# Kernel tuning notes

Measured on AMD Instinct MI355X. Metric: run time of the kernel, lower is better.

## Reference

```python
import jax, jax.numpy as jnp
import numpy as np

NUM_CLASSES = 4      # config.class_num (malaria stages)
N = 2048             # total nodes = source + target samples
S = 1024             # source_length
FEAT_IN = 25088      # VGG19 include_top=False -> 7*7*512 flattened
D_FC = 512           # Dense(512)
D_G1 = 512           # config.features_dim (GCNConv1 out)
D_G2 = 256           # config.GCN_hidderlayer_dim_num (GCNConv2 out)


def setup_inputs() -> dict:
    key = jax.random.key(0)
    ks = jax.random.split(key, 8)
    sc = lambda fan_in: np.float32(1.0 / np.sqrt(fan_in))
    return {
        "x": jax.random.normal(ks[0], (N, FEAT_IN), jnp.float32),
        "W_fc": jax.random.normal(ks[1], (FEAT_IN, D_FC), jnp.float32) * sc(FEAT_IN),
        "b_fc": jnp.zeros((D_FC,), jnp.float32),
        "W_g1": jax.random.normal(ks[2], (D_FC, D_G1), jnp.float32) * sc(D_FC),
        "b_g1": jnp.zeros((D_G1,), jnp.float32),
        "W_g2": jax.random.normal(ks[3], (D_G1, D_G2), jnp.float32) * sc(D_G1),
        "b_g2": jnp.zeros((D_G2,), jnp.float32),
        "source_labels": jax.random.randint(ks[4], (S,), 0, NUM_CLASSES),
        "source_length": S,
    }


def reference(x, W_fc, b_fc, W_g1, b_g1, W_g2, b_g2, source_labels, source_length):
    # fc after (omitted frozen) VGG19 backbone + flatten
    feats = x @ W_fc + b_fc                                   # [N, 512]

    # get_centers: per-class SUM of source features (no averaging, faithful)
    src = feats[:source_length]                               # [S, 512]
    centers = jax.ops.segment_sum(src, source_labels, num_segments=NUM_CLASSES)  # [C, 512]

    # per-target euclidean distance to each centroid + argmin
    # (argmin of squared distance == argmin of euclidean distance)
    tgt = feats[source_length:]                               # [T, 512]
    d2 = (jnp.sum(tgt * tgt, axis=1, keepdims=True)
          - 2.0 * (tgt @ centers.T)
          + jnp.sum(centers * centers, axis=1)[None, :])      # [T, C]
    target_labels = jnp.argmin(d2, axis=1)                    # [T] int

    # label-cluster graph: edge iff same label; source block forced to identity
    all_labels = jnp.concatenate([source_labels.astype(jnp.int32),
                                  target_labels.astype(jnp.int32)])
    adj = (all_labels[:, None] == all_labels[None, :]).astype(feats.dtype)  # [N, N]
    adj = adj.at[:source_length, :source_length].set(
        jnp.eye(source_length, dtype=feats.dtype))

    # add_self_loops(value=1) then symmetric gcn_filter D^-1/2 A D^-1/2
    A = adj + jnp.eye(N, dtype=feats.dtype)
    dinv = jax.lax.rsqrt(jnp.sum(A, axis=1))                  # [N]
    A_norm = dinv[:, None] * A * dinv[None, :]                # [N, N]

    # two GCN layers (spektral GCNConv: A_norm @ (X @ W) + b) with relu
    h = jax.nn.relu(A_norm @ (feats @ W_g1) + b_g1)           # [N, 512]
    h = jax.nn.relu(A_norm @ (h @ W_g2) + b_g2)               # [N, 256]
    return (h, A_norm, feats)
```

## Files before the change

kernel.cpp:

```cpp
#include <hip/hip_runtime.h>

#define NROWS 2048
#define SLEN  1024
#define FEAT  25088
#define DFC   512
#define DG1   512
#define DG2   256
#define CSPLIT 128

typedef __attribute__((ext_vector_type(8))) short short8;
typedef __attribute__((ext_vector_type(4))) float f32x4;

__device__ __forceinline__ unsigned short bfbits(float f) {
  unsigned int u = __float_as_uint(f);
  u += 0x7fffu + ((u >> 16) & 1u);
  return (unsigned short)(u >> 16);
}

__global__ void transpose_cvt_k(const float* __restrict__ src, unsigned short* __restrict__ dst,
                                int K, int Ncol) {
  __shared__ float tile[64][65];
  int kb = blockIdx.x * 64, nb = blockIdx.y * 64;
  int tx = threadIdx.x & 63, ty = threadIdx.x >> 6;
  #pragma unroll
  for (int i = ty; i < 64; i += 4)
    tile[i][tx] = src[(size_t)(kb + i) * Ncol + (nb + tx)];
  __syncthreads();
  #pragma unroll
  for (int i = ty; i < 64; i += 4)
    dst[(size_t)(nb + i) * K + (kb + tx)] = bfbits(tile[tx][i]);
}

template<bool AF32>
__global__ __launch_bounds__(256) void gemm_k(const void* __restrict__ Aptr,
    const unsigned short* __restrict__ BT, float* __restrict__ Cacc,
    int K, int Ncols, int tiles_n, int ksteps) {
  __shared__ unsigned short Al[128 * 40];
  __shared__ unsigned short Bl[128 * 40];
  int tid = threadIdx.x;
  int m0 = (blockIdx.x / tiles_n) * 128;
  int n0 = (blockIdx.x % tiles_n) * 128;
  int kbase = blockIdx.y * ksteps * 32;
  int wid = tid >> 6, lane = tid & 63;
  int wm = wid >> 1, wn = wid & 1;
  int lrow = lane & 15, lko = lane >> 4;

  f32x4 acc[4][4];
  #pragma unroll
  for (int i = 0; i < 4; i++)
    #pragma unroll
    for (int j = 0; j < 4; j++) acc[i][j] = (f32x4){0.f, 0.f, 0.f, 0.f};

  for (int t = 0; t < ksteps; ++t) {
    int k0 = kbase + t * 32;
    __syncthreads();
    if constexpr (AF32) {
      const float* A = (const float*)Aptr;
      #pragma unroll
      for (int i = 0; i < 4; i++) {
        int idx = tid + i * 256;
        int row = idx >> 3, kq = idx & 7;
        float4 v = *reinterpret_cast<const float4*>(A + (size_t)(m0 + row) * K + k0 + kq * 4);
        ushort4 u;
        u.x = bfbits(v.x); u.y = bfbits(v.y); u.z = bfbits(v.z); u.w = bfbits(v.w);
        *reinterpret_cast<ushort4*>(&Al[row * 40 + kq * 4]) = u;
      }
    } else {
      const unsigned short* A = (const unsigned short*)Aptr;
      #pragma unroll
      for (int i = 0; i < 2; i++) {
        int idx = tid + i * 256;
        int row = idx >> 2, kq = idx & 3;
        int4 v = *reinterpret_cast<const int4*>(A + (size_t)(m0 + row) * K + k0 + kq * 8);
        *reinterpret_cast<int4*>(&Al[row * 40 + kq * 8]) = v;
      }
    }
    #pragma unroll
    for (int i = 0; i < 2; i++) {
      int idx = tid + i * 256;
      int row = idx >> 2, kq = idx & 3;
      int4 v = *reinterpret_cast<const int4*>(BT + (size_t)(n0 + row) * K + k0 + kq * 8);
      *reinterpret_cast<int4*>(&Bl[row * 40 + kq * 8]) = v;
    }
    __syncthreads();
    short8 af[4], bfv[4];
    #pragma unroll
    for (int mi = 0; mi < 4; mi++)
      af[mi] = *reinterpret_cast<const short8*>(&Al[(wm * 64 + mi * 16 + lrow) * 40 + lko * 8]);
    #pragma unroll
    for (int ni = 0; ni < 4; ni++)
      bfv[ni] = *reinterpret_cast<const short8*>(&Bl[(wn * 64 + ni * 16 + lrow) * 40 + lko * 8]);
    #pragma unroll
    for (int mi = 0; mi < 4; mi++)
      #pragma unroll
      for (int ni = 0; ni < 4; ni++)
        acc[mi][ni] = __builtin_amdgcn_mfma_f32_16x16x32_bf16(af[mi], bfv[ni], acc[mi][ni], 0, 0, 0);
  }
  #pragma unroll
  for (int mi = 0; mi < 4; mi++)
    #pragma unroll
    for (int ni = 0; ni < 4; ni++)
      #pragma unroll
      for (int r = 0; r < 4; r++) {
        int row = m0 + wm * 64 + mi * 16 + lko * 4 + r;
        int col = n0 + wn * 64 + ni * 16 + lrow;
        atomicAdd(&Cacc[(size_t)row * Ncols + col], acc[mi][ni][r]);
      }
}

__global__ void feats_fin_k(const float* __restrict__ facc, const float* __restrict__ bfc,
                            float* __restrict__ outf, unsigned short* __restrict__ outbf) {
  int i = blockIdx.y;
  int n = blockIdx.x * 256 + threadIdx.x;
  float v = facc[(size_t)i * DFC + n] + bfc[n];
  outf[(size_t)i * DFC + n] = v;
  outbf[(size_t)i * DFC + n] = bfbits(v);
}

__global__ void seg_sum_part_k(const float* __restrict__ x, const int* __restrict__ slab,
                               float* __restrict__ sxp) {
  int k4 = blockIdx.x * 256 + threadIdx.x;
  if (k4 >= FEAT / 4) return;
  int k = k4 * 4;
  int i0 = blockIdx.y * 128, i1 = i0 + 128;
  float4 a0 = {0,0,0,0}, a1 = {0,0,0,0}, a2 = {0,0,0,0}, a3 = {0,0,0,0};
  #pragma unroll 4
  for (int i = i0; i < i1; i++) {
    float4 v = *reinterpret_cast<const float4*>(x + (size_t)i * FEAT + k);
    int c = slab[i];
    float m0 = (c == 0) ? 1.f : 0.f, m1 = (c == 1) ? 1.f : 0.f;
    float m2 = (c == 2) ? 1.f : 0.f, m3 = (c == 3) ? 1.f : 0.f;
    a0.x += m0 * v.x; a0.y += m0 * v.y; a0.z += m0 * v.z; a0.w += m0 * v.w;
    a1.x += m1 * v.x; a1.y += m1 * v.y; a1.z += m1 * v.z; a1.w += m1 * v.w;
    a2.x += m2 * v.x; a2.y += m2 * v.y; a2.z += m2 * v.z; a2.w += m2 * v.w;
    a3.x += m3 * v.x; a3.y += m3 * v.y; a3.z += m3 * v.z; a3.w += m3 * v.w;
  }
  size_t base = (size_t)blockIdx.y * 4 * FEAT;
  *reinterpret_cast<float4*>(sxp + base + 0 * FEAT + k) = a0;
  *reinterpret_cast<float4*>(sxp + base + 1 * FEAT + k) = a1;
  *reinterpret_cast<float4*>(sxp + base + 2 * FEAT + k) = a2;
  *reinterpret_cast<float4*>(sxp + base + 3 * FEAT + k) = a3;
}

__global__ void seg_sum_reduce_k(const float* __restrict__ sxp, float* __restrict__ sx) {
  int k4 = blockIdx.x * 256 + threadIdx.x;
  if (k4 >= FEAT / 4) return;
  int k = k4 * 4;
  int c = blockIdx.y;
  double s0 = 0, s1 = 0, s2 = 0, s3 = 0;
  #pragma unroll
  for (int p = 0; p < 8; p++) {
    float4 v = *reinterpret_cast<const float4*>(sxp + ((size_t)p * 4 + c) * FEAT + k);
    s0 += (double)v.x; s1 += (double)v.y; s2 += (double)v.z; s3 += (double)v.w;
  }
  float4 r; r.x = (float)s0; r.y = (float)s1; r.z = (float)s2; r.w = (float)s3;
  *reinterpret_cast<float4*>(sx + (size_t)c * FEAT + k) = r;
}

__global__ void count_src_k(const int* __restrict__ slab, int* __restrict__ cnt) {
  __shared__ int c[4];
  if (threadIdx.x < 4) c[threadIdx.x] = 0;
  __syncthreads();
  for (int i = threadIdx.x; i < SLEN; i += 256) atomicAdd(&c[slab[i]], 1);
  __syncthreads();
  if (threadIdx.x < 4) cnt[threadIdx.x] = c[threadIdx.x];
}

__global__ void centers_part_k(const float* __restrict__ sx, const float* __restrict__ W,
                               double* __restrict__ cpart) {
  int n = blockIdx.x * 64 + (threadIdx.x & 63);
  int cc = threadIdx.x >> 6;
  int kb = blockIdx.y * (FEAT / CSPLIT), ke = kb + FEAT / CSPLIT;
  const float* sr = sx + (size_t)cc * FEAT;
  double acc = 0.0;
  #pragma unroll 4
  for (int k = kb; k < ke; k++)
    acc += (double)sr[k] * (double)W[(size_t)k * DFC + n];
  cpart[((size_t)blockIdx.y * 4 + cc) * DFC + n] = acc;
}

__global__ void centers_reduce_k(const double* __restrict__ cpart, const float* __restrict__ bfc,
                                 const int* __restrict__ cntsrc, float* __restrict__ Cent) {
  int idx = blockIdx.x * 256 + threadIdx.x;
  int cc = idx >> 9, n = idx & 511;
  double s = 0.0;
  #pragma unroll 4
  for (int p = 0; p < CSPLIT; p++) s += cpart[((size_t)p * 4 + cc) * DFC + n];
  Cent[idx] = (float)(s + (double)cntsrc[cc] * (double)bfc[n]);
}

__global__ void wc_k(const float* __restrict__ W, const float* __restrict__ Cent,
                     float* __restrict__ wc) {
  __shared__ float cs[4 * DFC];
  for (int i = threadIdx.x; i < 4 * DFC; i += 256) cs[i] = Cent[i];
  __syncthreads();
  int k = blockIdx.x * 256 + threadIdx.x;
  if (k >= FEAT) return;
  const float* wr = W + (size_t)k * DFC;
  double a0 = 0, a1 = 0, a2 = 0, a3 = 0;
  #pragma unroll 2
  for (int n = 0; n < DFC; n += 4) {
    float4 w4 = *reinterpret_cast<const float4*>(wr + n);
    a0 += (double)w4.x * cs[0 * DFC + n] + (double)w4.y * cs[0 * DFC + n + 1]
        + (double)w4.z * cs[0 * DFC + n + 2] + (double)w4.w * cs[0 * DFC + n + 3];
    a1 += (double)w4.x * cs[1 * DFC + n] + (double)w4.y * cs[1 * DFC + n + 1]
        + (double)w4.z * cs[1 * DFC + n + 2] + (double)w4.w * cs[1 * DFC + n + 3];
    a2 += (double)w4.x * cs[2 * DFC + n] + (double)w4.y * cs[2 * DFC + n + 1]
        + (double)w4.z * cs[2 * DFC + n + 2] + (double)w4.w * cs[2 * DFC + n + 3];
    a3 += (double)w4.x * cs[3 * DFC + n] + (double)w4.y * cs[3 * DFC + n + 1]
        + (double)w4.z * cs[3 * DFC + n + 2] + (double)w4.w * cs[3 * DFC + n + 3];
  }
  float4 r; r.x = (float)a0; r.y = (float)a1; r.z = (float)a2; r.w = (float)a3;
  *reinterpret_cast<float4*>(wc + 4 * (size_t)k) = r;
}

__global__ void kj_k(const float* __restrict__ Cent, const float* __restrict__ bfc,
                     float* __restrict__ Kj) {
  int j = threadIdx.x >> 6, lane = threadIdx.x & 63;
  float cn = 0.f, bc = 0.f;
  for (int n = lane; n < DFC; n += 64) {
    float c = Cent[j * DFC + n];
    cn += c * c; bc += bfc[n] * c;
  }
  #pragma unroll
  for (int m = 32; m >= 1; m >>= 1) { cn += __shfl_xor(cn, m); bc += __shfl_xor(bc, m); }
  if (lane == 0) Kj[j] = cn - 2.f * bc;
}

__global__ void d2_labels_k(const float* __restrict__ x, const float* __restrict__ wc,
                            const float* __restrict__ Kj, int* __restrict__ tlab) {
  int row = blockIdx.x;
  int tid = threadIdx.x;
  const float* xr = x + (size_t)(SLEN + row) * FEAT;
  double a0 = 0, a1 = 0, a2 = 0, a3 = 0;
  #pragma unroll 2
  for (int k = tid; k < FEAT; k += 256) {
    float xv = xr[k];
    float4 w4 = *reinterpret_cast<const float4*>(wc + 4 * (size_t)k);
    a0 += (double)xv * w4.x; a1 += (double)xv * w4.y;
    a2 += (double)xv * w4.z; a3 += (double)xv * w4.w;
  }
  #pragma unroll
  for (int m = 32; m >= 1; m >>= 1) {
    a0 += __shfl_xor(a0, m); a1 += __shfl_xor(a1, m);
    a2 += __shfl_xor(a2, m); a3 += __shfl_xor(a3, m);
  }
  __shared__ double s[4][4];
  int wid = tid >> 6, lane = tid & 63;
  if (lane == 0) { s[wid][0] = a0; s[wid][1] = a1; s[wid][2] = a2; s[wid][3] = a3; }
  __syncthreads();
  if (tid == 0) {
    double t0 = s[0][0] + s[1][0] + s[2][0] + s[3][0];
    double t1 = s[0][1] + s[1][1] + s[2][1] + s[3][1];
    double t2 = s[0][2] + s[1][2] + s[2][2] + s[3][2];
    double t3 = s[0][3] + s[1][3] + s[2][3] + s[3][3];
    double s0 = (double)Kj[0] - 2.0 * t0;
    double s1 = (double)Kj[1] - 2.0 * t1;
    double s2 = (double)Kj[2] - 2.0 * t2;
    double s3 = (double)Kj[3] - 2.0 * t3;
    int bi = 0; double b = s0;
    if (s1 < b) { b = s1; bi = 1; }
    if (s2 < b) { b = s2; bi = 2; }
    if (s3 < b) { b = s3; bi = 3; }
    tlab[row] = bi;
  }
}

__global__ void finalize_labels_k(const int* __restrict__ slab, const int* __restrict__ tlab,
                                  const int* __restrict__ cntsrc, int* __restrict__ alllab,
                                  float* __restrict__ dinv) {
  __shared__ int ct[4];
  if (threadIdx.x < 4) ct[threadIdx.x] = 0;
  __syncthreads();
  for (int i = threadIdx.x; i < SLEN; i += 256) atomicAdd(&ct[tlab[i]], 1);
  __syncthreads();
  for (int i = threadIdx.x; i < NROWS; i += 256) {
    int lab = (i < SLEN) ? slab[i] : tlab[i - SLEN];
    alllab[i] = lab;
    float rs = (i < SLEN) ? (2.f + (float)ct[lab])
                          : (1.f + (float)cntsrc[lab] + (float)ct[lab]);
    dinv[i] = 1.f / sqrtf(rs);
  }
}

__global__ void anorm_k(const int* __restrict__ alllab, const float* __restrict__ dinv,
                        float* __restrict__ Aout) {
  int i = blockIdx.y;
  int j = blockIdx.x * 256 + threadIdx.x;
  int li = alllab[i], lj = alllab[j];
  float di = dinv[i], dj = dinv[j];
  float v;
  if (i == j) v = 2.f * di * dj;
  else if (i < SLEN && j < SLEN) v = 0.f;
  else v = (li == lj) ? di * dj : 0.f;
  Aout[(size_t)i * NROWS + j] = v;
}

__global__ void reduce_st_k(const float* __restrict__ Xacc, const int* __restrict__ alllab,
                            const float* __restrict__ dinv, float* __restrict__ ST, int D) {
  int n = blockIdx.x * 256 + threadIdx.x;
  int i0 = blockIdx.y * 32, i1 = i0 + 32;
  float s[4] = {0, 0, 0, 0}, tt[4] = {0, 0, 0, 0};
  for (int i = i0; i < i1; ++i) {
    float v = dinv[i] * Xacc[(size_t)i * D + n];
    int lab = alllab[i];
    bool src = i < SLEN;
    #pragma unroll
    for (int c = 0; c < 4; c++) {
      s[c]  += (src && lab == c) ? v : 0.f;
      tt[c] += (!src && lab == c) ? v : 0.f;
    }
  }
  #pragma unroll
  for (int c = 0; c < 4; c++) {
    atomicAdd(&ST[c * D + n], s[c]);
    atomicAdd(&ST[(4 + c) * D + n], tt[c]);
  }
}

__global__ void apply_prop_k(const float* __restrict__ Xacc, const float* __restrict__ ST,
                             const int* __restrict__ alllab, const float* __restrict__ dinv,
                             const float* __restrict__ bias, float* __restrict__ outf,
                             unsigned short* __restrict__ outbf, int D) {
  int i = blockIdx.y;
  int n = blockIdx.x * 256 + threadIdx.x;
  float dv = dinv[i];
  int lab = alllab[i];
  float xv = Xacc[(size_t)i * D + n];
  float z;
  if (i < SLEN) z = dv * (2.f * dv * xv + ST[(4 + lab) * D + n]);
  else          z = dv * (ST[lab * D + n] + ST[(4 + lab) * D + n] + dv * xv);
  z += bias[n];
  z = fmaxf(z, 0.f);
  if (outf)  outf[(size_t)i * D + n] = z;
  if (outbf) outbf[(size_t)i * D + n] = bfbits(z);
}

extern "C" void kernel_launch(void* const* d_in, const int* in_sizes, int n_in,
                              void* d_out, int out_size, void* d_ws, size_t ws_size,
                              hipStream_t stream) {
  const float* x    = (const float*)d_in[0];
  const float* Wfc  = (const float*)d_in[1];
  const float* bfc  = (const float*)d_in[2];
  const float* Wg1  = (const float*)d_in[3];
  const float* bg1  = (const float*)d_in[4];
  const float* Wg2  = (const float*)d_in[5];
  const float* bg2  = (const float*)d_in[6];
  const int*   slab = (const int*)d_in[7];

  float* out = (float*)d_out;
  float* out_h = out;
  float* out_A = out + 524288;
  float* out_f = out + 4718592;

  char* w = (char*)d_ws;
  unsigned short* wT   = (unsigned short*)(w);
  unsigned short* g1T  = (unsigned short*)(w + 25690112);
  unsigned short* g2T  = (unsigned short*)(w + 26214400);
  float* facc          = (float*)(w + 26476544);
  unsigned short* fbf  = (unsigned short*)(w + 30670848);
  float* x1acc         = (float*)(w + 32768000);
  unsigned short* h1bf = (unsigned short*)(w + 36962304);
  float* x2acc         = (float*)(w + 39059456);
  float* sx            = (float*)(w + 41156608);
  float* Cent          = (float*)(w + 41623552);
  float* wc            = (float*)(w + 41631744);
  float* Kj            = (float*)(w + 42033152);
  int*   tlab          = (int*)(w + 42033216);
  int*   alllab        = (int*)(w + 42037312);
  float* dinv          = (float*)(w + 42045504);
  int*   cntsrc        = (int*)(w + 42053696);
  float* ST1           = (float*)(w + 42053760);
  float* ST2           = (float*)(w + 42070144);

  float*  sxp     = (float*)(w + 26476544);
  double* cpart_d = (double*)(w + 39059456);

  hipMemsetAsync(facc,  0, (size_t)NROWS * DFC * 4, stream);
  hipMemsetAsync(x1acc, 0, (size_t)NROWS * DG1 * 4, stream);
  hipMemsetAsync(ST1,   0, 8 * DG1 * 4, stream);
  hipMemsetAsync(ST2,   0, 8 * DG2 * 4, stream);

  transpose_cvt_k<<<dim3(FEAT / 64, DFC / 64), 256, 0, stream>>>(Wfc, wT, FEAT, DFC);
  transpose_cvt_k<<<dim3(DFC / 64, DG1 / 64), 256, 0, stream>>>(Wg1, g1T, DFC, DG1);
  transpose_cvt_k<<<dim3(DG1 / 64, DG2 / 64), 256, 0, stream>>>(Wg2, g2T, DG1, DG2);

  gemm_k<true><<<dim3(16 * 4, 8), 256, 0, stream>>>(x, wT, facc, FEAT, DFC, 4, 98);
  feats_fin_k<<<dim3(DFC / 256, NROWS), 256, 0, stream>>>(facc, bfc, out_f, fbf);

  seg_sum_part_k<<<dim3(25, 8), 256, 0, stream>>>(x, slab, sxp);
  seg_sum_reduce_k<<<dim3(25, 4), 256, 0, stream>>>(sxp, sx);
  count_src_k<<<1, 256, 0, stream>>>(slab, cntsrc);
  centers_part_k<<<dim3(DFC / 64, CSPLIT), 256, 0, stream>>>(sx, Wfc, cpart_d);
  centers_reduce_k<<<dim3(4 * DFC / 256), 256, 0, stream>>>(cpart_d, bfc, cntsrc, Cent);
  wc_k<<<dim3(FEAT / 256), 256, 0, stream>>>(Wfc, Cent, wc);
  kj_k<<<1, 256, 0, stream>>>(Cent, bfc, Kj);
  d2_labels_k<<<dim3(NROWS - SLEN), 256, 0, stream>>>(x, wc, Kj, tlab);
  finalize_labels_k<<<1, 256, 0, stream>>>(slab, tlab, cntsrc, alllab, dinv);

  anorm_k<<<dim3(NROWS / 256, NROWS), 256, 0, stream>>>(alllab, dinv, out_A);

  gemm_k<false><<<dim3(16 * 4, 4), 256, 0, stream>>>(fbf, g1T, x1acc, DFC, DG1, 4, 4);
  reduce_st_k<<<dim3(DG1 / 256, 64), 256, 0, stream>>>(x1acc, alllab, dinv, ST1, DG1);
  apply_prop_k<<<dim3(DG1 / 256, NROWS), 256, 0, stream>>>(x1acc, ST1, alllab, dinv, bg1,
                                                           nullptr, h1bf, DG1);

  hipMemsetAsync(x2acc, 0, (size_t)NROWS * DG2 * 4, stream);
  gemm_k<false><<<dim3(16 * 2, 8), 256, 0, stream>>>(h1bf, g2T, x2acc, DG1, DG2, 2, 2);
  reduce_st_k<<<dim3(DG2 / 256, 64), 256, 0, stream>>>(x2acc, alllab, dinv, ST2, DG2);
  apply_prop_k<<<dim3(DG2 / 256, NROWS), 256, 0, stream>>>(x2acc, ST2, alllab, dinv, bg2,
                                                           out_h, nullptr, DG2);

  (void)in_sizes; (void)n_in; (void)out_size; (void)ws_size;
}
```

Before: 392.9 us.

## Use BK=64 swizzled LDS tiles with direct global-to-LDS loads in GEMM

The GEMM k-tile grows from 32 to 64 and moves to an XOR-swizzled 128-byte LDS row layout, which replaces the padded layout while keeping bank conflicts low. The bf16 operand tiles are now loaded with global_load_lds directly into LDS, skipping the trip through registers. Several smaller changes ride along: anorm writes float4 vectors, the segment-sum partials use 16 row splits instead of 8 with a relocated scratch buffer, and the x1acc memset moves later because that region now holds sxp. The larger tile halves the number of barriers per k, at the cost of more LDS per block and possible aliasing mistakes in the workspace.

```diff
diff --git a/kernel.cpp b/kernel.cpp
--- a/kernel.cpp
+++ b/kernel.cpp
@@ -17,6 +17,12 @@
   return (unsigned short)(u >> 16);
 }
 
+__device__ __forceinline__ void load_lds16(const void* g, void* l) {
+  __builtin_amdgcn_global_load_lds(
+      (const __attribute__((address_space(1))) unsigned int*)g,
+      (__attribute__((address_space(3))) unsigned int*)l, 16, 0, 0);
+}
+
 __global__ void transpose_cvt_k(const float* __restrict__ src, unsigned short* __restrict__ dst,
                                 int K, int Ncol) {
   __shared__ float tile[64][65];
@@ -35,12 +41,12 @@
 __global__ __launch_bounds__(256) void gemm_k(const void* __restrict__ Aptr,
     const unsigned short* __restrict__ BT, float* __restrict__ Cacc,
     int K, int Ncols, int tiles_n, int ksteps) {
-  __shared__ unsigned short Al[128 * 40];
-  __shared__ unsigned short Bl[128 * 40];
+  __shared__ unsigned short Al[128 * 64];
+  __shared__ unsigned short Bl[128 * 64];
   int tid = threadIdx.x;
   int m0 = (blockIdx.x / tiles_n) * 128;
   int n0 = (blockIdx.x % tiles_n) * 128;
-  int kbase = blockIdx.y * ksteps * 32;
+  int kbase = blockIdx.y * ksteps * 64;
   int wid = tid >> 6, lane = tid & 63;
   int wm = wid >> 1, wn = wid & 1;
   int lrow = lane & 15, lko = lane >> 4;
@@ -52,49 +58,64 @@
     for (int j = 0; j < 4; j++) acc[i][j] = (f32x4){0.f, 0.f, 0.f, 0.f};
 
   for (int t = 0; t < ksteps; ++t) {
-    int k0 = kbase + t * 32;
+    int k0 = kbase + t * 64;
     __syncthreads();
     if constexpr (AF32) {
       const float* A = (const float*)Aptr;
       #pragma unroll
-      for (int i = 0; i < 4; i++) {
-        int idx = tid + i * 256;
-        int row = idx >> 3, kq = idx & 7;
-        float4 v = *reinterpret_cast<const float4*>(A + (size_t)(m0 + row) * K + k0 + kq * 4);
-        ushort4 u;
-        u.x = bfbits(v.x); u.y = bfbits(v.y); u.z = bfbits(v.z); u.w = bfbits(v.w);
-        *reinterpret_cast<ushort4*>(&Al[row * 40 + kq * 4]) = u;
+      for (int j = 0; j < 4; j++) {
+        int ch = tid + j * 256;
+        int r = ch >> 3, c = ch & 7;
+        const float* g = A + (size_t)(m0 + r) * K + k0 + c * 8;
+        float4 v0 = *reinterpret_cast<const float4*>(g);
+        float4 v1 = *reinterpret_cast<const float4*>(g + 4);
+        unsigned int w0 = (unsigned)bfbits(v0.x) | ((unsigned)bfbits(v0.y) << 16);
+        unsigned int w1 = (unsigned)bfbits(v0.z) | ((unsigned)bfbits(v0.w) << 16);
+        unsigned int w2 = (unsigned)bfbits(v1.x) | ((unsigned)bfbits(v1.y) << 16);
+        unsigned int w3 = (unsigned)bfbits(v1.z) | ((unsigned)bfbits(v1.w) << 16);
+        int p = c ^ (r & 7);
+        int4 o; o.x = (int)w0; o.y = (int)w1; o.z = (int)w2; o.w = (int)w3;
+        *reinterpret_cast<int4*>((char*)Al + r * 128 + p * 16) = o;
       }
     } else {
       const unsigned short* A = (const unsigned short*)Aptr;
       #pragma unroll
-      for (int i = 0; i < 2; i++) {
-        int idx = tid + i * 256;
-        int row = idx >> 2, kq = idx & 3;
-        int4 v = *reinterpret_cast<const int4*>(A + (size_t)(m0 + row) * K + k0 + kq * 8);
-        *reinterpret_cast<int4*>(&Al[row * 40 + kq * 8]) = v;
+      for (int j = 0; j < 4; j++) {
+        int chb = j * 256 + wid * 64;
+        int ch = chb + lane;
+        int r = ch >> 3, c = (ch & 7) ^ (r & 7);
+        load_lds16(A + (size_t)(m0 + r) * K + k0 + c * 8, (char*)Al + chb * 16);
       }
     }
     #pragma unroll
-    for (int i = 0; i < 2; i++) {
-      int idx = tid + i * 256;
-      int row = idx >> 2, kq = idx & 3;
-      int4 v = *reinterpret_cast<const int4*>(BT + (size_t)(n0 + row) * K + k0 + kq * 8);
-      *reinterpret_cast<int4*>(&Bl[row * 40 + kq * 8]) = v;
+    for (int j = 0; j < 4; j++) {
+      int chb = j * 256 + wid * 64;
+      int ch = chb + lane;
+      int r = ch >> 3, c = (ch & 7) ^ (r & 7);
+      load_lds16(BT + (size_t)(n0 + r) * K + k0 + c * 8, (char*)Bl + chb * 16);
     }
     __syncthreads();
-    short8 af[4], bfv[4];
     #pragma unroll
-    for (int mi = 0; mi < 4; mi++)
-      af[mi] = *reinterpret_cast<const short8*>(&Al[(wm * 64 + mi * 16 + lrow) * 40 + lko * 8]);
-    #pragma unroll
-    for (int ni = 0; ni < 4; ni++)
-      bfv[ni] = *reinterpret_cast<const short8*>(&Bl[(wn * 64 + ni * 16 + lrow) * 40 + lko * 8]);
-    #pragma unroll
-    for (int mi = 0; mi < 4; mi++)
-      #pragma unroll
-      for (int ni = 0; ni < 4; ni++)
-        acc[mi][ni] = __builtin_amdgcn_mfma_f32_16x16x32_bf16(af[mi], bfv[ni], acc[mi][ni], 0, 0, 0);
+    for (int kk = 0; kk < 2; kk++) {
+      short8 af[4], bfv[4];
+      #pragma unroll
+      for (int mi = 0; mi < 4; mi++) {
+        int R = wm * 64 + mi * 16 + lrow;
+        int slot = ((kk << 2) | lko) ^ (lrow & 7);
+        af[mi] = *reinterpret_cast<const short8*>((char*)Al + R * 128 + slot * 16);
+      }
+      #pragma unroll
+      for (int ni = 0; ni < 4; ni++) {
+        int R = wn * 64 + ni * 16 + lrow;
+        int slot = ((kk << 2) | lko) ^ (lrow & 7);
+        bfv[ni] = *reinterpret_cast<const short8*>((char*)Bl + R * 128 + slot * 16);
+      }
+      #pragma unroll
+      for (int mi = 0; mi < 4; mi++)
+        #pragma unroll
+        for (int ni = 0; ni < 4; ni++)
+          acc[mi][ni] = __builtin_amdgcn_mfma_f32_16x16x32_bf16(af[mi], bfv[ni], acc[mi][ni], 0, 0, 0);
+    }
   }
   #pragma unroll
   for (int mi = 0; mi < 4; mi++)
@@ -122,7 +143,7 @@
   int k4 = blockIdx.x * 256 + threadIdx.x;
   if (k4 >= FEAT / 4) return;
   int k = k4 * 4;
-  int i0 = blockIdx.y * 128, i1 = i0 + 128;
+  int i0 = blockIdx.y * 64, i1 = i0 + 64;
   float4 a0 = {0,0,0,0}, a1 = {0,0,0,0}, a2 = {0,0,0,0}, a3 = {0,0,0,0};
   #pragma unroll 4
   for (int i = i0; i < i1; i++) {
@@ -149,7 +170,7 @@
   int c = blockIdx.y;
   double s0 = 0, s1 = 0, s2 = 0, s3 = 0;
   #pragma unroll
-  for (int p = 0; p < 8; p++) {
+  for (int p = 0; p < 16; p++) {
     float4 v = *reinterpret_cast<const float4*>(sxp + ((size_t)p * 4 + c) * FEAT + k);
     s0 += (double)v.x; s1 += (double)v.y; s2 += (double)v.z; s3 += (double)v.w;
   }
@@ -286,14 +307,25 @@
 __global__ void anorm_k(const int* __restrict__ alllab, const float* __restrict__ dinv,
                         float* __restrict__ Aout) {
   int i = blockIdx.y;
-  int j = blockIdx.x * 256 + threadIdx.x;
-  int li = alllab[i], lj = alllab[j];
-  float di = dinv[i], dj = dinv[j];
-  float v;
-  if (i == j) v = 2.f * di * dj;
-  else if (i < SLEN && j < SLEN) v = 0.f;
-  else v = (li == lj) ? di * dj : 0.f;
-  Aout[(size_t)i * NROWS + j] = v;
+  int j0 = (blockIdx.x * 256 + threadIdx.x) * 4;
+  int li = alllab[i];
+  float di = dinv[i];
+  int4 lj = *reinterpret_cast<const int4*>(alllab + j0);
+  float4 dj = *reinterpret_cast<const float4*>(dinv + j0);
+  int jj[4] = {lj.x, lj.y, lj.z, lj.w};
+  float dd[4] = {dj.x, dj.y, dj.z, dj.w};
+  float4 o;
+  float* op = &o.x;
+  #pragma unroll
+  for (int e = 0; e < 4; e++) {
+    int j = j0 + e;
+    float v;
+    if (i == j) v = 2.f * di * dd[e];
+    else if (i < SLEN && j < SLEN) v = 0.f;
+    else v = (li == jj[e]) ? di * dd[e] : 0.f;
+    op[e] = v;
+  }
+  *reinterpret_cast<float4*>(Aout + (size_t)i * NROWS + j0) = o;
 }
 
 __global__ void reduce_st_k(const float* __restrict__ Xacc, const int* __restrict__ alllab,
@@ -373,11 +405,10 @@
   float* ST1           = (float*)(w + 42053760);
   float* ST2           = (float*)(w + 42070144);
 
-  float*  sxp     = (float*)(w + 26476544);
+  float*  sxp     = (float*)(w + 32768000);
   double* cpart_d = (double*)(w + 39059456);
 
   hipMemsetAsync(facc,  0, (size_t)NROWS * DFC * 4, stream);
-  hipMemsetAsync(x1acc, 0, (size_t)NROWS * DG1 * 4, stream);
   hipMemsetAsync(ST1,   0, 8 * DG1 * 4, stream);
   hipMemsetAsync(ST2,   0, 8 * DG2 * 4, stream);
 
@@ -385,10 +416,10 @@
   transpose_cvt_k<<<dim3(DFC / 64, DG1 / 64), 256, 0, stream>>>(Wg1, g1T, DFC, DG1);
   transpose_cvt_k<<<dim3(DG1 / 64, DG2 / 64), 256, 0, stream>>>(Wg2, g2T, DG1, DG2);
 
-  gemm_k<true><<<dim3(16 * 4, 8), 256, 0, stream>>>(x, wT, facc, FEAT, DFC, 4, 98);
+  gemm_k<true><<<dim3(16 * 4, 8), 256, 0, stream>>>(x, wT, facc, FEAT, DFC, 4, 49);
   feats_fin_k<<<dim3(DFC / 256, NROWS), 256, 0, stream>>>(facc, bfc, out_f, fbf);
 
-  seg_sum_part_k<<<dim3(25, 8), 256, 0, stream>>>(x, slab, sxp);
+  seg_sum_part_k<<<dim3(25, 16), 256, 0, stream>>>(x, slab, sxp);
   seg_sum_reduce_k<<<dim3(25, 4), 256, 0, stream>>>(sxp, sx);
   count_src_k<<<1, 256, 0, stream>>>(slab, cntsrc);
   centers_part_k<<<dim3(DFC / 64, CSPLIT), 256, 0, stream>>>(sx, Wfc, cpart_d);
@@ -398,15 +429,16 @@
   d2_labels_k<<<dim3(NROWS - SLEN), 256, 0, stream>>>(x, wc, Kj, tlab);
   finalize_labels_k<<<1, 256, 0, stream>>>(slab, tlab, cntsrc, alllab, dinv);
 
-  anorm_k<<<dim3(NROWS / 256, NROWS), 256, 0, stream>>>(alllab, dinv, out_A);
-
-  gemm_k<false><<<dim3(16 * 4, 4), 256, 0, stream>>>(fbf, g1T, x1acc, DFC, DG1, 4, 4);
+  anorm_k<<<dim3(NROWS / 1024, NROWS), 256, 0, stream>>>(alllab, dinv, out_A);
+
+  hipMemsetAsync(x1acc, 0, (size_t)NROWS * DG1 * 4, stream);
+  gemm_k<false><<<dim3(16 * 4, 4), 256, 0, stream>>>(fbf, g1T, x1acc, DFC, DG1, 4, 2);
   reduce_st_k<<<dim3(DG1 / 256, 64), 256, 0, stream>>>(x1acc, alllab, dinv, ST1, DG1);
   apply_prop_k<<<dim3(DG1 / 256, NROWS), 256, 0, stream>>>(x1acc, ST1, alllab, dinv, bg1,
                                                            nullptr, h1bf, DG1);
 
   hipMemsetAsync(x2acc, 0, (size_t)NROWS * DG2 * 4, stream);
-  gemm_k<false><<<dim3(16 * 2, 8), 256, 0, stream>>>(h1bf, g2T, x2acc, DG1, DG2, 2, 2);
+  gemm_k<false><<<dim3(16 * 2, 8), 256, 0, stream>>>(h1bf, g2T, x2acc, DG1, DG2, 2, 1);
   reduce_st_k<<<dim3(DG2 / 256, 64), 256, 0, stream>>>(x2acc, alllab, dinv, ST2, DG2);
   apply_prop_k<<<dim3(DG2 / 256, NROWS), 256, 0, stream>>>(x2acc, ST2, alllab, dinv, bg2,
                                                            out_h, nullptr, DG2);
```

Result: faster. 381.5 us (-2.9%).
